# Optimization experiments

Hardware: AMD Instinct MI355X
Metric: run time of the kernel (lower is better)

## Reference

```python
import jax, jax.numpy as jnp
import numpy as np

NUM_HEADS = 12
NUM_GROUPS = 4
LN_EPS = 1e-12
NEG = -10000.0


def _ln(x, g, b):
    m = x.mean(-1, keepdims=True)
    v = ((x - m) ** 2).mean(-1, keepdims=True)
    return (x - m) * jax.lax.rsqrt(v + LN_EPS) * g + b


def _attention(h, ext_mask, Wattn, battn, ln):
    # h: [B,S,H]; ext_mask additive [B,1,1,S]; Wattn [4,H,H] = (q,k,v,o); battn [4,H]; ln [2,H]
    B, S, H = h.shape
    dh = H // NUM_HEADS
    q = (h @ Wattn[0] + battn[0]).reshape(B, S, NUM_HEADS, dh)
    k = (h @ Wattn[1] + battn[1]).reshape(B, S, NUM_HEADS, dh)
    v = (h @ Wattn[2] + battn[2]).reshape(B, S, NUM_HEADS, dh)
    scores = jnp.einsum('bqhd,bkhd->bhqk', q, k) * (1.0 / np.sqrt(dh)) + ext_mask
    p = jax.nn.softmax(scores, axis=-1)
    ctx = jnp.einsum('bhqk,bkhd->bqhd', p, v).reshape(B, S, H)
    # BertSelfOutput: dense + residual + LayerNorm
    return _ln(ctx @ Wattn[3] + battn[3] + h, ln[0], ln[1])


def _ffn(x, Wi, bi, Wo, bo, ln):
    # BertIntermediate (gelu) + BertOutput (dense + residual + LayerNorm)
    return _ln(jax.nn.gelu(x @ Wi + bi, approximate=False) @ Wo + bo + x, ln[0], ln[1])


def _bert_layer(h, ext_mask, Wattn, battn, ln_attn, Wi, bi, Wo, bo, ln_out):
    a = _attention(h, ext_mask, Wattn, battn, ln_attn)
    return _ffn(a, Wi, bi, Wo, bo, ln_out)


def _hier_attention(h, hier_mask, Wattn, battn, ln_attn, Wi, bi, Wo, bo, ln_out):
    # group masks [G,B,S]: 1 where hier_mask == group_id (ids 1..G)
    gids = jnp.arange(1, NUM_GROUPS + 1)
    masks = (hier_mask[None] == gids[:, None, None]).astype(h.dtype)  # [G,B,S]
    ext = (1.0 - masks)[:, :, None, None, :] * NEG                    # [G,B,1,1,S]
    # one full BertLayer per group (vectorized over G instead of batch concat)
    outs = jax.vmap(lambda m: _bert_layer(h, m, Wattn, battn, ln_attn, Wi, bi, Wo, bo, ln_out))(ext)  # [G,B,S,H]
    return jnp.sum(outs * masks[..., None], axis=0)


def reference(hidden_states, attention_mask, main_Wattn, main_battn, main_ln_attn,
              main_Wi, main_bi, main_Wo, main_bo, main_ln_out,
              hier_Wattn, hier_battn, hier_ln_attn, hier_Wi, hier_bi, hier_Wo,
              hier_bo, hier_ln_out, hier_mask):
    attn_out = _attention(hidden_states, attention_mask, main_Wattn, main_battn, main_ln_attn)
    hier_out = _hier_attention(hidden_states, hier_mask, hier_Wattn, hier_battn,
                               hier_ln_attn, hier_Wi, hier_bi, hier_Wo, hier_bo, hier_ln_out)
    combined = attn_out + hier_out
    return _ffn(combined, main_Wi, main_bi, main_Wo, main_bo, main_ln_out)


def setup_inputs() -> dict:
    key = jax.random.key(0)
    ks = jax.random.split(key, 20)
    B, S, H, F = 8, 512, 768, 3072
    W = 0.02  # weight init scale

    def layer_params(k):
        kk = jax.random.split(k, 8)
        return dict(
            Wattn=jax.random.normal(kk[0], (4, H, H), jnp.float32) * W,
            battn=jax.random.normal(kk[1], (4, H), jnp.float32) * W,
            ln_attn=jnp.stack([1.0 + jax.random.normal(kk[2], (H,), jnp.float32) * W,
                               jax.random.normal(kk[3], (H,), jnp.float32) * W]),
            Wi=jax.random.normal(kk[4], (H, F), jnp.float32) * W,
            bi=jax.random.normal(kk[5], (F,), jnp.float32) * W,
            Wo=jax.random.normal(kk[6], (F, H), jnp.float32) * W,
            bo=jax.random.normal(kk[7], (H,), jnp.float32) * W,
            ln_out=jnp.stack([1.0 + jax.random.normal(kk[2], (H,), jnp.float32) * W,
                              jax.random.normal(kk[3], (H,), jnp.float32) * W]),
        )

    main = layer_params(ks[0])
    hier = layer_params(ks[1])
    inp = {
        'hidden_states': jax.random.normal(ks[2], (B, S, H), jnp.float32),
        'attention_mask': jnp.zeros((B, 1, 1, S), jnp.float32),
        'hier_mask': jax.random.randint(ks[3], (B, S), 0, 5).astype(jnp.int64),
    }
    for name, p in (('main', main), ('hier', hier)):
        for k2, v in p.items():
            inp[f'{name}_{k2}'] = v
    return inp
```

## Files before the change

### kernel.cpp

```cpp
#include <hip/hip_runtime.h>
#include <hip/hip_bf16.h>

#define DI __device__ __forceinline__

typedef __attribute__((ext_vector_type(4))) float  f32x4;
typedef __attribute__((ext_vector_type(8))) short  s16x8;
typedef __attribute__((ext_vector_type(4))) short  s16x4;
typedef __attribute__((ext_vector_type(8))) __bf16 bf16x8;

DI short f2bf(float f) {
  union { float f; unsigned u; } v; v.f = f;
  unsigned r = v.u + 0x7fffu + ((v.u >> 16) & 1u);
  return (short)(r >> 16);
}
DI float bf2f(short s) {
  union { unsigned u; float f; } v; v.u = ((unsigned)(unsigned short)s) << 16;
  return v.f;
}

DI f32x4 mfma16(s16x8 a, s16x8 b, f32x4 c) {
  return __builtin_amdgcn_mfma_f32_16x16x32_bf16(
      __builtin_bit_cast(bf16x8, a), __builtin_bit_cast(bf16x8, b), c, 0, 0, 0);
}

typedef const __attribute__((address_space(1))) unsigned* gas_p;
typedef __attribute__((address_space(3))) unsigned* las_p;
DI void gload16(const void* g, void* l) {
  __builtin_amdgcn_global_load_lds((gas_p)g, (las_p)l, 16, 0, 0);
}

template<int N> DI void wait_vmcnt() {
  asm volatile("s_waitcnt vmcnt(%0)" :: "n"(N) : "memory");
}

__global__ __launch_bounds__(256) void cast_bf16(const float* __restrict__ x,
                                                 short* __restrict__ y) {
  const int i = (blockIdx.x * 256 + threadIdx.x) * 4;
  const float4 t = *(const float4*)&x[i];
  s16x4 o;
  o[0] = f2bf(t.x); o[1] = f2bf(t.y); o[2] = f2bf(t.z); o[3] = f2bf(t.w);
  *(s16x4*)&y[i] = o;
}

struct TJob { const float* src; short* dst; int K, N, tile0; };
struct TJobs { TJob j[12]; };

__global__ __launch_bounds__(256) void transpose_w(TJobs jobs) {
  __shared__ float T[32][33];
  const int t = blockIdx.x;
  int ji = 0;
#pragma unroll
  for (int i = 1; i < 12; ++i) if (jobs.j[i].tile0 <= t) ji = i;
  const float* src = jobs.j[ji].src;
  short* dst = jobs.j[ji].dst;
  const int K = jobs.j[ji].K, N = jobs.j[ji].N;
  const int lt = t - jobs.j[ji].tile0;
  const int tn = N >> 5;
  const int n0 = (lt % tn) << 5, k0 = (lt / tn) << 5;
  const int tid = threadIdx.x;
#pragma unroll
  for (int i = 0; i < 4; ++i) {
    const int c = i * 256 + tid, r = c >> 5, cc = c & 31;
    T[cc][r] = src[(long long)(k0 + r) * N + n0 + cc];
  }
  __syncthreads();
#pragma unroll
  for (int i = 0; i < 4; ++i) {
    const int c = i * 256 + tid, r = c >> 5, cc = c & 31;
    dst[(long long)(n0 + r) * K + k0 + cc] = f2bf(T[r][cc]);
  }
}

template<int BM, int BN, int WM, int WN, int EPI>
__global__ __launch_bounds__(256) void gemm_bt(
    const short* __restrict__ A, int lda, long long sA,
    const short* __restrict__ B, int ldb, long long sB,
    void* __restrict__ Cv, int ldc,
    long long cOuter, int cInner, int cStride,
    const float* __restrict__ bias, const float* __restrict__ bias2,
    int K, int nSplit,
    short* __restrict__ vtOut) {
  constexpr int BK = 32;
  constexpr int WNW = BN / WN;
  constexpr int MFR = WM / 16, NFR = WN / 16;
  constexpr int ALD = BM / 64;
  constexpr int BLD = BN / 64;
  constexpr int LPT = ALD + BLD;

  __shared__ short As[3][BM * BK];
  __shared__ short Bs[3][BN * BK];

  const int z = blockIdx.z;
  const int zb = z / nSplit, zs = z - zb * nSplit;
  const short* Ab = A + (long long)zb * sA + (long long)zs * K;
  const short* Bb = B + (long long)zb * sB + (long long)zs * K;
  const long long cOff = (long long)(z / cInner) * cOuter + (long long)(z % cInner) * cStride;
  const float* bi = (bias2 && zb) ? bias2 : bias;

  const int bm = blockIdx.x * BM;
  const int bn = blockIdx.y * BN;
  const int tid = threadIdx.x;
  const int wave = tid >> 6, lane = tid & 63;
  const int wm = (wave / WNW) * WM;
  const int wn = (wave % WNW) * WN;
  const int l16 = lane & 15, lk = lane >> 4;

  const int scol = ((tid & 3) ^ ((tid >> 3) & 3)) * 8;
  const short* aBase = Ab + (long long)(bm + (tid >> 2)) * lda + scol;
  const short* bBase = Bb + (long long)(bn + (tid >> 2)) * ldb + scol;
  const int ldsOff = wave * 64 * 8;
  const int rslot = (lk ^ ((l16 >> 1) & 3)) * 8;

  f32x4 acc[MFR][NFR] = {};

  auto stage = [&](int buf, int kt) {
#pragma unroll
    for (int i = 0; i < ALD; ++i)
      gload16(aBase + kt + (long long)(i * 64) * lda, &As[buf][i * 2048 + ldsOff]);
#pragma unroll
    for (int i = 0; i < BLD; ++i)
      gload16(bBase + kt + (long long)(i * 64) * ldb, &Bs[buf][i * 2048 + ldsOff]);
  };

  const int nt = K / BK;
  stage(0, 0);
  if (nt > 1) stage(1, BK);
  int cur = 0;
  for (int t = 0; t < nt; ++t) {
    if (t + 1 < nt) wait_vmcnt<LPT>();
    else            wait_vmcnt<0>();
    __builtin_amdgcn_s_barrier();
    s16x8 af[MFR], bfr[NFR];
#pragma unroll
    for (int mi = 0; mi < MFR; ++mi)
      af[mi] = *(const s16x8*)&As[cur][(wm + mi * 16 + l16) * BK + rslot];
#pragma unroll
    for (int ni = 0; ni < NFR; ++ni)
      bfr[ni] = *(const s16x8*)&Bs[cur][(wn + ni * 16 + l16) * BK + rslot];
#pragma unroll
    for (int mi = 0; mi < MFR; ++mi)
#pragma unroll
      for (int ni = 0; ni < NFR; ++ni)
        acc[mi][ni] = mfma16(bfr[ni], af[mi], acc[mi][ni]);
    if (t + 2 < nt) {
      const int nb = cur + 2 >= 3 ? cur - 1 : cur + 2;
      stage(nb, (t + 2) * BK);
    }
    cur = (cur + 1 == 3) ? 0 : cur + 1;
  }

#pragma unroll
  for (int mi = 0; mi < MFR; ++mi) {
    const int row = bm + wm + mi * 16 + l16;
#pragma unroll
    for (int ni = 0; ni < NFR; ++ni) {
      const int col = bn + wn + ni * 16 + lk * 4;
      const long long idx = cOff + (long long)row * ldc + col;
      f32x4 bv = {};
      if (EPI != 2 && bi) bv = *(const f32x4*)&bi[col];
      f32x4 v = acc[mi][ni] + bv;
      if constexpr (EPI == 0 || EPI == 2 || EPI == 3) {
        s16x4 o;
#pragma unroll
        for (int r = 0; r < 4; ++r) o[r] = f2bf(v[r]);
        *(s16x4*)&((short*)Cv)[idx] = o;
        if constexpr (EPI == 3) {
          if (col >= 1536) {
            const int b = row >> 9, s = row & 511;
            const int hc = col - 1536;
            const int bh = b * 12 + (hc >> 6);
            const int d0 = hc & 63;
            short* vp = vtOut + (long long)zb * 3145728 +
                        (long long)bh * 32768 + (long long)d0 * 512 + s;
#pragma unroll
            for (int r = 0; r < 4; ++r) vp[r * 512] = o[r];
          }
        }
      } else {
        s16x4 o;
#pragma unroll
        for (int r = 0; r < 4; ++r) {
          const float g = 0.5f * v[r] * (1.f + erff(v[r] * 0.70710678118654752f));
          o[r] = f2bf(g);
        }
        *(s16x4*)&((short*)Cv)[idx] = o;
      }
    }
  }
}

template<int HIER>
__global__ __launch_bounds__(256) void attn_scores(
    const short* __restrict__ QKV,
    const float* __restrict__ amask,
    const int* __restrict__ hmask,
    short* __restrict__ P) {
  __shared__ short Qs[32 * 64];
  __shared__ short Ks[256 * 64];
  __shared__ float red[32 * 4];
  __shared__ int   hm[512];

  const int bh = blockIdx.y;
  const int b = bh / 12, hh = bh % 12;
  const int q0 = blockIdx.x * 32;
  const int tid = threadIdx.x;
  const int wave = tid >> 6, lane = tid & 63;
  const int l16 = lane & 15, lk = lane >> 4;
  const long long rowbase = (long long)(b * 512) * 2304 + hh * 64;

  {
    const int c = tid;
    const int d8 = ((c & 7) ^ ((c >> 3) & 7)) * 8;
    gload16(QKV + rowbase + (long long)(q0 + (c >> 3)) * 2304 + d8,
            &Qs[wave * 64 * 8]);
  }
  if constexpr (HIER) {
    for (int i = tid; i < 512; i += 256) hm[i] = hmask[b * 512 + i];
  }

  f32x4 acc[2][8] = {};
#pragma unroll
  for (int kc = 0; kc < 2; ++kc) {
    if (kc) __syncthreads();
#pragma unroll
    for (int i = 0; i < 8; ++i) {
      const int c = i * 256 + tid;
      const int d8 = ((c & 7) ^ ((c >> 3) & 7)) * 8;
      gload16(QKV + rowbase + 768 + (long long)(kc * 256 + (c >> 3)) * 2304 + d8,
              &Ks[(i * 256 + wave * 64) * 8]);
    }
    __syncthreads();
#pragma unroll
    for (int ks = 0; ks < 2; ++ks) {
      s16x8 af[2], bfr[4];
#pragma unroll
      for (int mi = 0; mi < 2; ++mi)
        af[mi] = *(const s16x8*)&Qs[(mi * 16 + l16) * 64 +
                                    (((ks * 4 + lk) ^ (l16 & 7)) * 8)];
#pragma unroll
      for (int ni = 0; ni < 4; ++ni)
        bfr[ni] = *(const s16x8*)&Ks[(wave * 64 + ni * 16 + l16) * 64 +
                                     (((ks * 4 + lk) ^ (l16 & 7)) * 8)];
#pragma unroll
      for (int mi = 0; mi < 2; ++mi)
#pragma unroll
        for (int ni = 0; ni < 4; ++ni)
          acc[mi][kc * 4 + ni] = mfma16(af[mi], bfr[ni], acc[mi][kc * 4 + ni]);
    }
  }

  int gq[2][4];
  if constexpr (HIER) {
#pragma unroll
    for (int mi = 0; mi < 2; ++mi)
#pragma unroll
      for (int r = 0; r < 4; ++r)
        gq[mi][r] = hm[q0 + mi * 16 + lk * 4 + r];
  }
  int hk[8]; float am[8];
#pragma unroll
  for (int nig = 0; nig < 8; ++nig) {
    const int col = (nig >> 2) * 256 + wave * 64 + (nig & 3) * 16 + l16;
    if constexpr (HIER) hk[nig] = hm[col];
    else                am[nig] = amask[b * 512 + col];
  }
#pragma unroll
  for (int mi = 0; mi < 2; ++mi)
#pragma unroll
    for (int nig = 0; nig < 8; ++nig)
#pragma unroll
      for (int r = 0; r < 4; ++r) {
        float v = acc[mi][nig][r] * 0.125f;
        if constexpr (HIER) v += (hk[nig] == gq[mi][r]) ? 0.f : -10000.f;
        else                v += am[nig];
        acc[mi][nig][r] = v;
      }

  float mx[2][4];
#pragma unroll
  for (int mi = 0; mi < 2; ++mi)
#pragma unroll
    for (int r = 0; r < 4; ++r) {
      float m = acc[mi][0][r];
#pragma unroll
      for (int nig = 1; nig < 8; ++nig) m = fmaxf(m, acc[mi][nig][r]);
#pragma unroll
      for (int d = 1; d < 16; d <<= 1) m = fmaxf(m, __shfl_xor(m, d));
      mx[mi][r] = m;
      red[(mi * 16 + lk * 4 + r) * 4 + wave] = m;
    }
  __syncthreads();
#pragma unroll
  for (int mi = 0; mi < 2; ++mi)
#pragma unroll
    for (int r = 0; r < 4; ++r) {
      const int q = mi * 16 + lk * 4 + r;
      mx[mi][r] = fmaxf(fmaxf(red[q * 4], red[q * 4 + 1]),
                        fmaxf(red[q * 4 + 2], red[q * 4 + 3]));
    }
  __syncthreads();

  float sm[2][4];
#pragma unroll
  for (int mi = 0; mi < 2; ++mi)
#pragma unroll
    for (int r = 0; r < 4; ++r) {
      float s = 0.f;
#pragma unroll
      for (int nig = 0; nig < 8; ++nig) {
        const float e = __expf(acc[mi][nig][r] - mx[mi][r]);
        acc[mi][nig][r] = e;
        s += e;
      }
#pragma unroll
      for (int d = 1; d < 16; d <<= 1) s += __shfl_xor(s, d);
      sm[mi][r] = s;
      red[(mi * 16 + lk * 4 + r) * 4 + wave] = s;
    }
  __syncthreads();
#pragma unroll
  for (int mi = 0; mi < 2; ++mi)
#pragma unroll
    for (int r = 0; r < 4; ++r) {
      const int q = mi * 16 + lk * 4 + r;
      sm[mi][r] = 1.f / (red[q * 4] + red[q * 4 + 1] + red[q * 4 + 2] + red[q * 4 + 3]);
    }

  const long long Pbase = (long long)bh * 512 * 512;
#pragma unroll
  for (int mi = 0; mi < 2; ++mi)
#pragma unroll
    for (int nig = 0; nig < 8; ++nig) {
      const int col = (nig >> 2) * 256 + wave * 64 + (nig & 3) * 16 + l16;
#pragma unroll
      for (int r = 0; r < 4; ++r) {
        const int q = mi * 16 + lk * 4 + r;
        P[Pbase + (long long)(q0 + q) * 512 + col] = f2bf(acc[mi][nig][r] * sm[mi][r]);
      }
    }
}

template<int NS, int MODE>
__global__ __launch_bounds__(256) void ln_red(
    const short* __restrict__ part, const float* __restrict__ bias,
    const float* __restrict__ res, const float* __restrict__ ln,
    float* __restrict__ outf, short* __restrict__ outb,
    const int* __restrict__ hmask) {
  constexpr long long SP = 4096LL * 768;
  const int row = blockIdx.x * 4 + (threadIdx.x >> 6);
  const int lane = threadIdx.x & 63;
  const long long rb = (long long)row * 768;
  float v[12];
  float s = 0.f;
#pragma unroll
  for (int i = 0; i < 3; ++i) {
    const int c4 = lane + (i << 6);
    float4 t = ((const float4*)(res + rb))[c4];
    const float4 bv = ((const float4*)bias)[c4];
    t.x += bv.x; t.y += bv.y; t.z += bv.z; t.w += bv.w;
#pragma unroll
    for (int ss = 0; ss < NS; ++ss) {
      const s16x4 p = *(const s16x4*)&part[ss * SP + rb + c4 * 4];
      t.x += bf2f(p[0]); t.y += bf2f(p[1]); t.z += bf2f(p[2]); t.w += bf2f(p[3]);
    }
    v[i * 4 + 0] = t.x; v[i * 4 + 1] = t.y; v[i * 4 + 2] = t.z; v[i * 4 + 3] = t.w;
    s += t.x + t.y + t.z + t.w;
  }
#pragma unroll
  for (int d = 1; d < 64; d <<= 1) s += __shfl_xor(s, d);
  const float mean = s * (1.f / 768.f);
  float vs = 0.f;
#pragma unroll
  for (int i = 0; i < 12; ++i) { const float dv = v[i] - mean; vs += dv * dv; }
#pragma unroll
  for (int d = 1; d < 64; d <<= 1) vs += __shfl_xor(vs, d);
  const float rstd = rsqrtf(vs * (1.f / 768.f) + 1e-12f);
  int keep = 1;
  if constexpr (MODE == 2) keep = (hmask[row] != 0);
#pragma unroll
  for (int i = 0; i < 3; ++i) {
    const int c4 = lane + (i << 6);
    const float4 g = ((const float4*)ln)[c4];
    const float4 be = ((const float4*)(ln + 768))[c4];
    const float gg[4] = {g.x, g.y, g.z, g.w}, bb[4] = {be.x, be.y, be.z, be.w};
    float resv[4];
#pragma unroll
    for (int j = 0; j < 4; ++j) {
      float yv = (v[i * 4 + j] - mean) * rstd * gg[j] + bb[j];
      if constexpr (MODE == 2) {
        const float a = outf[rb + c4 * 4 + j];
        yv = a + (keep ? yv : 0.f);
      }
      resv[j] = yv;
    }
    float4 of; of.x = resv[0]; of.y = resv[1]; of.z = resv[2]; of.w = resv[3];
    ((float4*)(outf + rb))[c4] = of;
    if constexpr (MODE >= 1) {
      s16x4 ob;
#pragma unroll
      for (int j = 0; j < 4; ++j) ob[j] = f2bf(resv[j]);
      *(s16x4*)&outb[rb + c4 * 4] = ob;
    }
  }
}

extern "C" void kernel_launch(void* const* d_in, const int* in_sizes, int n_in,
                              void* d_out, int out_size, void* d_ws, size_t ws_size,
                              hipStream_t stream) {
  (void)in_sizes; (void)n_in; (void)out_size; (void)ws_size;
  const float* h      = (const float*)d_in[0];
  const float* amask  = (const float*)d_in[1];
  const int*   hmask  = (const int*)d_in[2];
  const float* mWattn = (const float*)d_in[3];
  const float* mbattn = (const float*)d_in[4];
  const float* mlnA   = (const float*)d_in[5];
  const float* mWi    = (const float*)d_in[6];
  const float* mbi    = (const float*)d_in[7];
  const float* mWo    = (const float*)d_in[8];
  const float* mbo    = (const float*)d_in[9];
  const float* mlnO   = (const float*)d_in[10];
  const float* hWattn = (const float*)d_in[11];
  const float* hbattn = (const float*)d_in[12];
  const float* hlnA   = (const float*)d_in[13];
  const float* hWi    = (const float*)d_in[14];
  const float* hbi    = (const float*)d_in[15];
  const float* hWo    = (const float*)d_in[16];
  const float* hbo    = (const float*)d_in[17];
  const float* hlnO   = (const float*)d_in[18];
  float* out = (float*)d_out;

  char* ws = (char*)d_ws;
  size_t off = 0;
  auto alloc = [&](size_t bytes) {
    void* p = ws + off;
    off += (bytes + 255) & ~(size_t)255;
    return p;
  };
  const long long SC  = 4096LL * 768;
  const long long SC3 = 4096LL * 2304;
  short* wq2  = (short*)alloc(2ull * 2304 * 768 * 2);
  short* wo2  = (short*)alloc(2ull * 768 * 768 * 2);
  short* wi_m = (short*)alloc(3072ull * 768 * 2);
  short* wi_h = (short*)alloc(3072ull * 768 * 2);
  short* wf_m = (short*)alloc(768ull * 3072 * 2);
  short* wf_h = (short*)alloc(768ull * 3072 * 2);
  short* hbf  = (short*)alloc(4096ull * 768 * 2);
  short* qkv2 = (short*)alloc(2ull * SC3 * 2);
  short* vt2  = (short*)alloc(2ull * 96 * 64 * 512 * 2);
  short* Pb   = (short*)alloc(96ull * 512 * 512 * 2);
  short* ctxb = (short*)alloc(2ull * 4096 * 768 * 2);
  float* pre1 = (float*)alloc(4096ull * 768 * 4);
  float* attn = (float*)alloc(4096ull * 768 * 4);
  short* abf  = (short*)alloc(4096ull * 768 * 2);
  short* cbf  = (short*)alloc(4096ull * 768 * 2);
  short* mid  = qkv2;
  short* part = Pb;

  cast_bf16<<<dim3(3072), dim3(256), 0, stream>>>(h, hbf);

  TJobs tj; int tile = 0; int nj = 0;
  auto add = [&](const float* s, short* d, int K, int N) {
    tj.j[nj].src = s; tj.j[nj].dst = d; tj.j[nj].K = K; tj.j[nj].N = N; tj.j[nj].tile0 = tile;
    tile += (K / 32) * (N / 32); nj++;
  };
  const long long WQ = 2304LL * 768;
  add(mWattn,              wq2,                768, 768);
  add(mWattn + 589824,     wq2 + 589824,       768, 768);
  add(mWattn + 2 * 589824, wq2 + 2 * 589824,   768, 768);
  add(mWattn + 3 * 589824, wo2,                768, 768);
  add(mWi,                 wi_m,               768, 3072);
  add(mWo,                 wf_m,               3072, 768);
  add(hWattn,              wq2 + WQ,           768, 768);
  add(hWattn + 589824,     wq2 + WQ + 589824,  768, 768);
  add(hWattn + 2 * 589824, wq2 + WQ + 2 * 589824, 768, 768);
  add(hWattn + 3 * 589824, wo2 + 589824,       768, 768);
  add(hWi,                 wi_h,               768, 3072);
  add(hWo,                 wf_h,               3072, 768);
  transpose_w<<<dim3(tile), dim3(256), 0, stream>>>(tj);

  gemm_bt<128, 128, 64, 64, 3><<<dim3(32, 18, 2), dim3(256), 0, stream>>>(
      hbf, 768, 0, wq2, 768, WQ, qkv2, 2304, SC3, 1, 0,
      mbattn, hbattn, 768, 1, vt2);

  auto attn_tail = [&](int hier, short* ctx) {
    const short* qkv = qkv2 + (long long)hier * SC3;
    const short* vt  = vt2 + (long long)hier * 3145728;
    if (hier)
      attn_scores<1><<<dim3(16, 96), dim3(256), 0, stream>>>(qkv, amask, hmask, Pb);
    else
      attn_scores<0><<<dim3(16, 96), dim3(256), 0, stream>>>(qkv, amask, hmask, Pb);
    gemm_bt<64, 64, 32, 32, 0><<<dim3(8, 1, 96), dim3(256), 0, stream>>>(
        Pb, 512, 262144LL, vt, 512, 32768LL,
        ctx, 768, 512LL * 768, 12, 64, nullptr, nullptr, 512, 1, nullptr);
  };
  attn_tail(0, ctxb);
  attn_tail(1, ctxb + SC);

  gemm_bt<128, 128, 64, 64, 2><<<dim3(32, 6, 4), dim3(256), 0, stream>>>(
      ctxb, 768, SC, wo2, 768, 589824LL, part, 768, SC, 1, 0,
      nullptr, nullptr, 384, 2, nullptr);
  ln_red<2, 0><<<dim3(1024), dim3(256), 0, stream>>>(
      part, mbattn + 2304, h, mlnA, attn, nullptr, nullptr);
  ln_red<2, 1><<<dim3(1024), dim3(256), 0, stream>>>(
      part + 2 * SC, hbattn + 2304, h, hlnA, pre1, abf, nullptr);

  gemm_bt<128, 128, 64, 64, 1><<<dim3(32, 24, 1), dim3(256), 0, stream>>>(
      abf, 768, 0, wi_h, 768, 0, mid, 3072, 0, 1, 0, hbi, nullptr, 768, 1, nullptr);
  gemm_bt<128, 128, 64, 64, 2><<<dim3(32, 6, 4), dim3(256), 0, stream>>>(
      mid, 3072, 0, wf_h, 3072, 0, part, 768, SC, 1, 0, nullptr, nullptr, 768, 4, nullptr);
  ln_red<4, 2><<<dim3(1024), dim3(256), 0, stream>>>(
      part, hbo, pre1, hlnO, attn, cbf, hmask);

  gemm_bt<128, 128, 64, 64, 1><<<dim3(32, 24, 1), dim3(256), 0, stream>>>(
      cbf, 768, 0, wi_m, 768, 0, mid, 3072, 0, 1, 0, mbi, nullptr, 768, 1, nullptr);
  gemm_bt<128, 128, 64, 64, 2><<<dim3(32, 6, 4), dim3(256), 0, stream>>>(
      mid, 3072, 0, wf_m, 3072, 0, part, 768, SC, 1, 0, nullptr, nullptr, 768, 4, nullptr);
  ln_red<4, 0><<<dim3(1024), dim3(256), 0, stream>>>(
      part, mbo, attn, mlnO, out, nullptr, nullptr);
}
```

Baseline: 354.3 us.

## Fuse softmax probabilities with PV matmul inside attention kernel

The attention scores kernel now keeps the normalized probabilities in shared memory (reusing the K buffer with an XOR swizzle) and multiplies them by the transposed V directly with MFMA, writing the context output. This removes the global round trip of the 512x512 bf16 probability matrix per head and the separate batched GEMM launch for each branch. In exchange, the V operand is streamed from global memory without LDS staging, and the kernel carries more work and an extra barrier.

New measurement: 333.6 us. -5.8%, faster.

```diff
diff --git a/kernel.cpp b/kernel.cpp
--- a/kernel.cpp
+++ b/kernel.cpp
@@ -190,11 +190,12 @@
 }
 
 template<int HIER>
-__global__ __launch_bounds__(256) void attn_scores(
+__global__ __launch_bounds__(256) void attn_fused(
     const short* __restrict__ QKV,
     const float* __restrict__ amask,
     const int* __restrict__ hmask,
-    short* __restrict__ P) {
+    const short* __restrict__ Vt,
+    short* __restrict__ ctx) {
   __shared__ short Qs[32 * 64];
   __shared__ short Ks[256 * 64];
   __shared__ float red[32 * 4];
@@ -326,7 +327,6 @@
       sm[mi][r] = 1.f / (red[q * 4] + red[q * 4 + 1] + red[q * 4 + 2] + red[q * 4 + 3]);
     }
 
-  const long long Pbase = (long long)bh * 512 * 512;
 #pragma unroll
   for (int mi = 0; mi < 2; ++mi)
 #pragma unroll
@@ -335,9 +335,33 @@
 #pragma unroll
       for (int r = 0; r < 4; ++r) {
         const int q = mi * 16 + lk * 4 + r;
-        P[Pbase + (long long)(q0 + q) * 512 + col] = f2bf(acc[mi][nig][r] * sm[mi][r]);
+        const int swz = (((col >> 3) ^ (q & 7)) << 3) | (col & 7);
+        Ks[q * 512 + swz] = f2bf(acc[mi][nig][r] * sm[mi][r]);
       }
     }
+  __syncthreads();
+
+  const short* vb = Vt + (long long)bh * 32768 + (wave * 16 + l16) * 512 + lk * 8;
+  f32x4 pacc[2] = {};
+  s16x8 vn = *(const s16x8*)vb;
+#pragma unroll
+  for (int s = 0; s < 16; ++s) {
+    const s16x8 bfr = vn;
+    if (s + 1 < 16) vn = *(const s16x8*)(vb + (s + 1) * 32);
+    const int ch = ((s * 4 + lk) ^ (l16 & 7)) * 8;
+    const s16x8 af0 = *(const s16x8*)&Ks[l16 * 512 + ch];
+    const s16x8 af1 = *(const s16x8*)&Ks[(16 + l16) * 512 + ch];
+    pacc[0] = mfma16(bfr, af0, pacc[0]);
+    pacc[1] = mfma16(bfr, af1, pacc[1]);
+  }
+#pragma unroll
+  for (int mi = 0; mi < 2; ++mi) {
+    s16x4 o;
+#pragma unroll
+    for (int r = 0; r < 4; ++r) o[r] = f2bf(pacc[mi][r]);
+    *(s16x4*)&ctx[(long long)(b * 512 + q0 + mi * 16 + l16) * 768 +
+                  hh * 64 + wave * 16 + lk * 4] = o;
+  }
 }
 
 template<int NS, int MODE>
@@ -482,19 +506,10 @@
       hbf, 768, 0, wq2, 768, WQ, qkv2, 2304, SC3, 1, 0,
       mbattn, hbattn, 768, 1, vt2);
 
-  auto attn_tail = [&](int hier, short* ctx) {
-    const short* qkv = qkv2 + (long long)hier * SC3;
-    const short* vt  = vt2 + (long long)hier * 3145728;
-    if (hier)
-      attn_scores<1><<<dim3(16, 96), dim3(256), 0, stream>>>(qkv, amask, hmask, Pb);
-    else
-      attn_scores<0><<<dim3(16, 96), dim3(256), 0, stream>>>(qkv, amask, hmask, Pb);
-    gemm_bt<64, 64, 32, 32, 0><<<dim3(8, 1, 96), dim3(256), 0, stream>>>(
-        Pb, 512, 262144LL, vt, 512, 32768LL,
-        ctx, 768, 512LL * 768, 12, 64, nullptr, nullptr, 512, 1, nullptr);
-  };
-  attn_tail(0, ctxb);
-  attn_tail(1, ctxb + SC);
+  attn_fused<0><<<dim3(16, 96), dim3(256), 0, stream>>>(
+      qkv2, amask, hmask, vt2, ctxb);
+  attn_fused<1><<<dim3(16, 96), dim3(256), 0, stream>>>(
+      qkv2 + SC3, amask, hmask, vt2 + 3145728, ctxb + SC);
 
   gemm_bt<128, 128, 64, 64, 2><<<dim3(32, 6, 4), dim3(256), 0, stream>>>(
       ctxb, 768, SC, wo2, 768, 589824LL, part, 768, SC, 1, 0,
```
